# Kernel tuning notes

Measured on AMD Instinct MI355X. Metric: run time of the kernel, lower is better.

The kernel has to match this reference:

```python
import jax, jax.numpy as jnp
import numpy as np

B, S, D, H, MEL = 64, 512, 512, 8, 80
HD = D // H  # head dim


def _lstm_cell(x, h, c, w_ih, w_hh, b_ih, b_hh):
    # torch gate order: i, f, g, o
    gates = x @ w_ih.T + h @ w_hh.T + b_ih + b_hh
    i, f, g, o = jnp.split(gates, 4, axis=-1)
    c = jax.nn.sigmoid(f) * c + jax.nn.sigmoid(i) * jnp.tanh(g)
    h = jax.nn.sigmoid(o) * jnp.tanh(c)
    return h, c


def setup_inputs() -> dict:
    key = jax.random.key(0)
    ks = jax.random.split(key, 24)
    s = 0.05
    inp = {"encoder_output": jax.random.normal(ks[0], (B, S, D), jnp.float32)}
    # MultiheadAttention params (torch layout: in_proj [3D, D])
    inp["attn_in_w"] = jax.random.normal(ks[1], (3 * D, D), jnp.float32) * s
    inp["attn_in_b"] = jax.random.normal(ks[2], (3 * D,), jnp.float32) * s
    inp["attn_out_w"] = jax.random.normal(ks[3], (D, D), jnp.float32) * s
    inp["attn_out_b"] = jax.random.normal(ks[4], (D,), jnp.float32) * s
    # LSTM1 (2 layers)
    names = [("l1_w_ih0", (4 * D, D)), ("l1_w_hh0", (4 * D, D)), ("l1_b_ih0", (4 * D,)), ("l1_b_hh0", (4 * D,)),
             ("l1_w_ih1", (4 * D, D)), ("l1_w_hh1", (4 * D, D)), ("l1_b_ih1", (4 * D,)), ("l1_b_hh1", (4 * D,)),
             ("l2_w_ih", (4 * D, D)), ("l2_w_hh", (4 * D, D)), ("l2_b_ih", (4 * D,)), ("l2_b_hh", (4 * D,)),
             ("proj_w", (MEL, D)), ("proj_b", (MEL,))]
    for i, (n, shp) in enumerate(names):
        inp[n] = jax.random.normal(ks[5 + i], shp, jnp.float32) * s
    return inp


def reference(encoder_output, attn_in_w, attn_in_b, attn_out_w, attn_out_b,
              l1_w_ih0, l1_w_hh0, l1_b_ih0, l1_b_hh0,
              l1_w_ih1, l1_w_hh1, l1_b_ih1, l1_b_hh1,
              l2_w_ih, l2_w_hh, l2_b_ih, l2_b_hh, proj_w, proj_b):
    b, s, d = encoder_output.shape
    max_len = s * 5
    wq, wk, wv = jnp.split(attn_in_w, 3, axis=0)
    bq, bk, bv = jnp.split(attn_in_b, 3, axis=0)
    # Precompute K, V over encoder output: [B, S, H, HD]
    K = (encoder_output @ wk.T + bk).reshape(b, s, H, HD)
    V = (encoder_output @ wv.T + bv).reshape(b, s, H, HD)
    scale = 1.0 / np.sqrt(HD)

    def attend(x):  # x: [B, D] single-token query
        q = ((x @ wq.T + bq) * scale).reshape(b, H, HD)
        scores = jnp.einsum('bhd,bshd->bhs', q, K)
        w = jax.nn.softmax(scores, axis=-1)
        ctx = jnp.einsum('bhs,bshd->bhd', w, V).reshape(b, d)
        return ctx @ attn_out_w.T + attn_out_b

    zeros = jnp.zeros((b, d), encoder_output.dtype)
    carry0 = (zeros, zeros, zeros, zeros, zeros, zeros, zeros)

    def step(carry, _):
        h10, c10, h11, c11, h2, c2, dec_in = carry
        h10, c10 = _lstm_cell(dec_in, h10, c10, l1_w_ih0, l1_w_hh0, l1_b_ih0, l1_b_hh0)
        h11, c11 = _lstm_cell(h10, h11, c11, l1_w_ih1, l1_w_hh1, l1_b_ih1, l1_b_hh1)
        attn_out = attend(h11)
        h2, c2 = _lstm_cell(attn_out, h2, c2, l2_w_ih, l2_w_hh, l2_b_ih, l2_b_hh)
        out = h2 @ proj_w.T + proj_b  # [B, MEL]
        return (h10, c10, h11, c11, h2, c2, h2), out

    _, ys = jax.lax.scan(step, carry0, None, length=max_len)
    return jnp.transpose(ys, (1, 0, 2))  # [B, max_len, MEL]
```

## Files before the change

### kernel.cpp

```cpp
#include <hip/hip_runtime.h>
#include <hip/hip_bf16.h>
#include <hip/hip_fp8.h>

#define DEV_INLINE __device__ __forceinline__

typedef __attribute__((ext_vector_type(8))) short bf16x8;
typedef __attribute__((ext_vector_type(4))) float f32x4;
typedef __attribute__((ext_vector_type(2))) float f32x2;
typedef __attribute__((ext_vector_type(4))) unsigned int u32x4;
typedef unsigned long long ull;

constexpr int Bc = 64, Sc = 512, Dc = 512, Hc = 8, HDc = 64, MELc = 80, Tc = 2560;
constexpr int OUTSTRIDE = Tc * MELc;

constexpr size_t SZ_KP8 = 64ull * 8 * 512 * 64;
constexpr size_t SZ_VP  = 64ull * 8 * 512 * 64 * 2;
constexpr size_t SZ_PL  = 128ull * 2048 * 16;
constexpr size_t OFF_KP8 = 0;
constexpr size_t OFF_VP  = OFF_KP8 + SZ_KP8;
constexpr size_t OFF_PL0 = OFF_VP + SZ_VP;
constexpr size_t OFF_PL1 = OFF_PL0 + SZ_PL;
constexpr size_t OFF_PL2 = OFF_PL1 + SZ_PL;
constexpr size_t OFF_PWQ = OFF_PL2 + SZ_PL;
constexpr size_t OFF_PP  = OFF_PWQ + 524288;
constexpr size_t OFF_BL0 = OFF_PP + 81920;
constexpr size_t OFF_BL1 = OFF_BL0 + 8192;
constexpr size_t OFF_BL2 = OFF_BL1 + 8192;
constexpr size_t OFF_B2E = OFF_BL2 + 8192;
constexpr size_t OFF_W2E = OFF_B2E + 8192;
constexpr size_t OFF_WOT = OFF_W2E + 2097152;
constexpr size_t OFF_ACT = OFF_WOT + 1048576;
constexpr size_t OFF_FLG = OFF_ACT + 524288;

constexpr unsigned DYN_LDS = 121088;

DEV_INLINE float bf2f(short s) { return __uint_as_float(((unsigned)(unsigned short)s) << 16); }
DEV_INLINE short f2bf(float f) { union { __hip_bfloat16 h; short s; } u; u.h = __float2bfloat16(f); return u.s; }
DEV_INLINE float sig_f(float x) { return 1.0f / (1.0f + __expf(-x)); }
DEV_INLINE float tanh_f(float x) {
  float ax = fabsf(x);
  float e = __expf(fminf(2.0f * ax, 80.0f));
  float r = 1.0f - 2.0f / (e + 1.0f);
  return copysignf(r, x);
}
DEV_INLINE bf16x8 cvt8(const float* p) {
  bf16x8 r;
#pragma unroll
  for (int i = 0; i < 8; ++i) r[i] = f2bf(p[i]);
  return r;
}
DEV_INLINE float fp8tof(unsigned v) {
  __hip_fp8_e4m3 t; t.__x = (__hip_fp8_storage_t)v; return (float)t;
}

template <bool HI>
DEV_INLINE f32x2 cvt2_fp8(unsigned w) {
#if defined(__has_builtin) && __has_builtin(__builtin_amdgcn_cvt_pk_f32_fp8)
  return __builtin_amdgcn_cvt_pk_f32_fp8(w, HI);
#else
  unsigned b = HI ? (w >> 16) : w;
  f32x2 r; r[0] = fp8tof(b & 0xFFu); r[1] = fp8tof((b >> 8) & 0xFFu);
  return r;
#endif
}

DEV_INLINE ull ld_dev_u64(const void* p) {
  return __hip_atomic_load((const ull*)p, __ATOMIC_RELAXED, __HIP_MEMORY_SCOPE_AGENT);
}
DEV_INLINE void st_dev_u64(void* p, ull v) {
  __hip_atomic_store((ull*)p, v, __ATOMIC_RELAXED, __HIP_MEMORY_SCOPE_AGENT);
}
DEV_INLINE bf16x8 ld_frag(const __hip_bfloat16* p) {
  union { bf16x8 v; ull u[2]; } r;
  r.u[0] = ld_dev_u64(p);
  r.u[1] = ld_dev_u64((const char*)p + 8);
  return r.v;
}

__global__ __launch_bounds__(256) void gemm_setup(const float* __restrict__ A,
                                                  const float* __restrict__ Bt,
                                                  const float* __restrict__ bias,
                                                  __hip_bfloat16* __restrict__ dst,
                                                  unsigned char* __restrict__ dst8,
                                                  int mode) {
  int tid = threadIdx.x, lane = tid & 63, wv = tid >> 6;
  int m0 = blockIdx.y * 64 + wv * 16;
  int nb = blockIdx.x * 64;
  int mrow = m0 + (lane & 15);
  int kb = (lane >> 4) * 8;
  f32x4 acc0 = {0,0,0,0}, acc1 = {0,0,0,0}, acc2 = {0,0,0,0}, acc3 = {0,0,0,0};
  const float* arow = A + (size_t)mrow * 512 + kb;
  const float* b0r = Bt + (size_t)(nb + 0 * 16 + (lane & 15)) * 512 + kb;
  const float* b1r = Bt + (size_t)(nb + 1 * 16 + (lane & 15)) * 512 + kb;
  const float* b2r = Bt + (size_t)(nb + 2 * 16 + (lane & 15)) * 512 + kb;
  const float* b3r = Bt + (size_t)(nb + 3 * 16 + (lane & 15)) * 512 + kb;
  for (int kk = 0; kk < 16; ++kk) {
    bf16x8 af = cvt8(arow + kk * 32);
    acc0 = __builtin_amdgcn_mfma_f32_16x16x32_bf16(af, cvt8(b0r + kk * 32), acc0, 0, 0, 0);
    acc1 = __builtin_amdgcn_mfma_f32_16x16x32_bf16(af, cvt8(b1r + kk * 32), acc1, 0, 0, 0);
    acc2 = __builtin_amdgcn_mfma_f32_16x16x32_bf16(af, cvt8(b2r + kk * 32), acc2, 0, 0, 0);
    acc3 = __builtin_amdgcn_mfma_f32_16x16x32_bf16(af, cvt8(b3r + kk * 32), acc3, 0, 0, 0);
  }
  int col16 = lane & 15, r0 = (lane >> 4) * 4;
  f32x4 accs[4] = {acc0, acc1, acc2, acc3};
#pragma unroll
  for (int nt = 0; nt < 4; ++nt) {
    int n = nb + nt * 16 + col16;
#pragma unroll
    for (int r = 0; r < 4; ++r) {
      int m = m0 + r0 + r;
      float v = accs[nt][r];
      if (mode == 0) {
        v += bias[n];
        int bb = m >> 9, s = m & 511, h = n >> 6, d = n & 63;
        dst[(((size_t)(bb * 8 + h) * 512 + s) * 64) + d] = __float2bfloat16(v);
      } else if (mode == 2) {
        v += bias[n];
        int bb = m >> 9, s = m & 511, h = n >> 6, d = n & 63;
        __hip_fp8_e4m3 q(v);
        dst8[(((size_t)(bb * 8 + h) * 512 + s) * 64) + d] = (unsigned char)q.__x;
      } else {
        dst[(size_t)m * 512 + n] = __float2bfloat16(v);
      }
    }
  }
}

__global__ __launch_bounds__(256) void transpose512(const float* __restrict__ in, float* __restrict__ out) {
  __shared__ float tl[32][33];
  int x = threadIdx.x & 31, ty = threadIdx.x >> 5;
  int bx = blockIdx.x * 32, by = blockIdx.y * 32;
#pragma unroll
  for (int r = 0; r < 4; ++r) tl[ty + r * 8][x] = in[(size_t)(by + ty + r * 8) * 512 + bx + x];
  __syncthreads();
#pragma unroll
  for (int r = 0; r < 4; ++r) out[(size_t)(bx + ty + r * 8) * 512 + by + x] = tl[x][ty + r * 8];
}

__global__ __launch_bounds__(256) void b2eff_k(const float* __restrict__ w2ih, const float* __restrict__ bout,
                                               const float* __restrict__ bih, const float* __restrict__ bhh,
                                               float* __restrict__ dst) {
  int g = blockIdx.x * 256 + threadIdx.x;
  float acc = bih[g] + bhh[g];
  const float* row = w2ih + (size_t)g * 512;
  for (int k = 0; k < 512; ++k) acc += row[k] * bout[k];
  dst[g] = acc;
}

__global__ __launch_bounds__(256) void pack_lstm(const float* __restrict__ lo_f32,
                                                 const __hip_bfloat16* __restrict__ lo_bf16,
                                                 const float* __restrict__ hi_f32,
                                                 const float* __restrict__ b1, const float* __restrict__ b2,
                                                 const float* __restrict__ b_pre,
                                                 __hip_bfloat16* __restrict__ dst, float* __restrict__ bias_out,
                                                 int mode) {
  int u = blockIdx.x, tid = threadIdx.x;
  for (int rep = 0; rep < 8; ++rep) {
    int slot = rep * 256 + tid;
    int kk = slot >> 6, lane = slot & 63;
    int n16 = lane & 15, gate = n16 >> 2, jj = n16 & 3;
    int srow = gate * 512 + u * 4 + jj;
    int k = kk * 32 + (lane >> 4) * 8;
    __hip_bfloat16 tmp[8];
    if (k < 512) {
      if (mode == 0) {
#pragma unroll
        for (int i = 0; i < 8; ++i) tmp[i] = __float2bfloat16(lo_f32[(size_t)srow * 512 + k + i]);
      } else {
#pragma unroll
        for (int i = 0; i < 8; ++i) tmp[i] = lo_bf16[(size_t)srow * 512 + k + i];
      }
    } else {
#pragma unroll
      for (int i = 0; i < 8; ++i) tmp[i] = __float2bfloat16(hi_f32[(size_t)srow * 512 + (k - 512) + i]);
    }
    *(uint4*)(dst + ((size_t)u * 2048 + slot) * 8) = *(uint4*)tmp;
  }
  if (tid < 16) {
    int gate = tid >> 2, jj = tid & 3;
    int srow = gate * 512 + u * 4 + jj;
    bias_out[u * 16 + tid] = (mode == 0) ? (b1[srow] + b2[srow]) : b_pre[srow];
  }
}

__global__ __launch_bounds__(256) void pack_wq(const float* __restrict__ wq, __hip_bfloat16* __restrict__ dst) {
  int h = blockIdx.x, tid = threadIdx.x;
  for (int rep = 0; rep < 16; ++rep) {
    int slot = rep * 256 + tid;
    int nt = slot >> 10, kk = (slot >> 6) & 15, lane = slot & 63;
    int srow = h * 64 + nt * 16 + (lane & 15);
    int k = kk * 32 + (lane >> 4) * 8;
    __hip_bfloat16 tmp[8];
#pragma unroll
    for (int i = 0; i < 8; ++i) tmp[i] = __float2bfloat16(wq[(size_t)srow * 512 + k + i]);
    *(uint4*)(dst + ((size_t)h * 4096 + slot) * 8) = *(uint4*)tmp;
  }
}

struct DecParams {
  const float* attn_in_b;
  const float* proj_b;
  const float* proj_w;
  const uint4* packL0; const uint4* packL1; const uint4* packL2;
  const float* biasL0; const float* biasL1; const float* biasL2;
  const uint4* packWq;
  const unsigned char* Kp8; const __hip_bfloat16* Vp;
  __hip_bfloat16* h10b; __hip_bfloat16* h11b; __hip_bfloat16* h2b; __hip_bfloat16* ctxb;
  ull* actbase;
  unsigned* flags;
  float* out;
};

constexpr ull WD_TICKS = 200000000ull;

DEV_INLINE unsigned* ctrp(unsigned* f, int g, int s, int h) {
  return f + 32 + (((g << 2) + s) * 2 + h) * 32;
}

DEV_INLINE void publish_ctr(unsigned* c, int tid) {
  __builtin_amdgcn_s_waitcnt(0);
  __syncthreads();
  if (tid == 0)
    (void)__hip_atomic_fetch_add(c, 1u, __ATOMIC_RELAXED, __HIP_MEMORY_SCOPE_AGENT);
}

DEV_INLINE bool wait_ctr(unsigned* c, unsigned target, ull t0, int* sbail) {
  for (;;) {
    unsigned v = (unsigned)__builtin_amdgcn_readfirstlane(
        (int)__hip_atomic_load(c, __ATOMIC_RELAXED, __HIP_MEMORY_SCOPE_AGENT));
    if (v >= target) return true;
    if (__builtin_amdgcn_s_memrealtime() - t0 > WD_TICKS) { *sbail = 1; return false; }
    __builtin_amdgcn_s_sleep(1);
  }
}

DEV_INLINE void prefetch_hi(bf16x8* pf, const __hip_bfloat16* hi, int g, int lane, int wv) {
  if (wv >= 2) {
    const __hip_bfloat16* p = hi + (size_t)(g * 32 + (wv & 1) * 16 + (lane & 15)) * 512 + (lane >> 4) * 8;
#pragma unroll
    for (int kk = 0; kk < 16; ++kk) pf[kk] = ld_frag(p + kk * 32);
  }
}

DEV_INLINE bool lstm_stage(int tid, int g, int wgl,
                           const uint4* wlds, const float* bias,
                           const __hip_bfloat16* lo, const bf16x8* pf,
                           float* cstate, __hip_bfloat16* hc,
                           float* pred, ull* st64,
                           unsigned* c_lo, unsigned* c_hi, unsigned target,
                           ull t0, int* sbail) {
  const int lane = tid & 63, wv = tid >> 6, mt = wv & 1, kh = wv >> 1;
  f32x4 acc = {0,0,0,0};
  if (kh == 0) {
    const __hip_bfloat16* pA = lo + (size_t)(g * 32 + mt * 16 + (lane & 15)) * 512 + (lane >> 4) * 8;
    if (wait_ctr(c_lo, target, t0, sbail)) {
#pragma unroll
      for (int kk = 0; kk < 8; ++kk) {
        bf16x8 a = ld_frag(pA + kk * 32);
        bf16x8 b = *(const bf16x8*)(wlds + kk * 64 + lane);
        acc = __builtin_amdgcn_mfma_f32_16x16x32_bf16(a, b, acc, 0, 0, 0);
      }
      if (wait_ctr(c_hi, target, t0, sbail)) {
#pragma unroll
        for (int kk = 8; kk < 16; ++kk) {
          bf16x8 a = ld_frag(pA + kk * 32);
          bf16x8 b = *(const bf16x8*)(wlds + kk * 64 + lane);
          acc = __builtin_amdgcn_mfma_f32_16x16x32_bf16(a, b, acc, 0, 0, 0);
        }
      }
    }
  } else {
#pragma unroll
    for (int kk = 0; kk < 16; ++kk) {
      bf16x8 b = *(const bf16x8*)(wlds + (16 + kk) * 64 + lane);
      acc = __builtin_amdgcn_mfma_f32_16x16x32_bf16(pf[kk], b, acc, 0, 0, 0);
    }
  }
#pragma unroll
  for (int r = 0; r < 4; ++r) pred[wv * 256 + lane * 4 + r] = acc[r];
  __syncthreads();
  if (*sbail) return false;
  if (tid < 128) {
    int bl = tid >> 2, j = tid & 3;
    int mt2 = bl >> 4, qd = (bl & 15) >> 2, reg = bl & 3;
    const float* p0 = pred + mt2 * 256;
    const float* p1 = pred + (2 + mt2) * 256;
    int l0 = qd * 16;
    float gi = p0[(l0 + j) * 4 + reg]      + p1[(l0 + j) * 4 + reg]      + bias[j];
    float gf = p0[(l0 + 4 + j) * 4 + reg]  + p1[(l0 + 4 + j) * 4 + reg]  + bias[4 + j];
    float gg = p0[(l0 + 8 + j) * 4 + reg]  + p1[(l0 + 8 + j) * 4 + reg]  + bias[8 + j];
    float go = p0[(l0 + 12 + j) * 4 + reg] + p1[(l0 + 12 + j) * 4 + reg] + bias[12 + j];
    float c = cstate[tid & 127];
    c = sig_f(gf) * c + sig_f(gi) * tanh_f(gg);
    float h = sig_f(go) * tanh_f(c);
    cstate[tid & 127] = c;
    ((unsigned short*)st64)[tid] = (unsigned short)f2bf(h);
  }
  __syncthreads();
  if (tid < 32)
    st_dev_u64(hc + (size_t)(g * 32 + tid) * 512 + wgl * 4, st64[tid]);
  return true;
}

DEV_INLINE void proj_spread(int tid, int g, int wgl, const float* pw, const float* pb,
                            const __hip_bfloat16* h2in, float* outp) {
  const int lane = tid & 63, pr = tid >> 6;
#pragma unroll
  for (int r = 0; r < 5; ++r) {
    int P = wgl * 20 + r * 4 + pr;
    int b = P / 80, m = P - b * 80;
    bf16x8 hv = ld_frag(h2in + (size_t)(g * 32 + b) * 512 + lane * 8);
    const f32x4* w4 = (const f32x4*)(pw + (size_t)m * 512 + lane * 8);
    f32x4 wa = w4[0], wb = w4[1];
    float acc = bf2f(hv[0]) * wa[0] + bf2f(hv[1]) * wa[1] + bf2f(hv[2]) * wa[2] + bf2f(hv[3]) * wa[3]
              + bf2f(hv[4]) * wb[0] + bf2f(hv[5]) * wb[1] + bf2f(hv[6]) * wb[2] + bf2f(hv[7]) * wb[3];
#pragma unroll
    for (int off = 32; off; off >>= 1) acc += __shfl_xor(acc, off);
    if (lane == 0) outp[(size_t)(g * 32 + b) * OUTSTRIDE + m] = acc + pb[m];
  }
}

__global__ __launch_bounds__(256, 1) void decoder_main(DecParams P) {
  extern __shared__ char smem[];
  uint4* wL0 = (uint4*)smem;
  uint4* wL1 = wL0 + 2048;
  uint4* wL2 = wL1 + 2048;
  ull*   st64 = (ull*)(wL2 + 2048);
  float* pred = (float*)(st64 + 32);
  float* qls  = pred + 1024;
  float* sco  = qls + 1088;
  float* red  = sco + 1024;
  float* cst  = red + 2048;
  float* smx  = cst + 384;
  float* ssum = smx + 4;
  float* sinv = ssum + 4;
  int*   sbail = (int*)(sinv + 2);

  const int wg = blockIdx.x, tid = threadIdx.x;
  const int lane = tid & 63, wv = tid >> 6;
  const int g = wg >> 7;
  const int wgl = wg & 127;
  const int myhalf = wgl >> 6;
  const int hh = wgl >> 4;
  const int b0g = (wgl & 15) * 2;
  const int bblk = b0g & ~15;

  const ull t0 = __builtin_amdgcn_s_memrealtime();
  unsigned* F = P.flags;

  {
    const uint4* s0 = P.packL0 + (size_t)wgl * 2048;
    const uint4* s1 = P.packL1 + (size_t)wgl * 2048;
    const uint4* s2 = P.packL2 + (size_t)wgl * 2048;
    for (int i = tid; i < 2048; i += 256) { wL0[i] = s0[i]; wL1[i] = s1[i]; wL2[i] = s2[i]; }
  }
  if (tid == 0) *sbail = 0;
  if (tid < 128) { cst[tid] = 0.0f; cst[128 + tid] = 0.0f; cst[256 + tid] = 0.0f; }
  st_dev_u64(P.actbase + (size_t)wg * 256 + tid, 0ull);
  __syncthreads();
  publish_ctr(F, tid);
  if (!wait_ctr(F, 256u, t0, sbail)) goto bail;
  __syncthreads();

  for (int t = 0; t < Tc; ++t) {
    const int cur = t & 1, pv = cur ^ 1;
    const unsigned tgtP = 64u * (unsigned)t;
    const unsigned tgtC = 64u * (unsigned)(t + 1);
    __hip_bfloat16* h10c = P.h10b + cur * 32768; __hip_bfloat16* h10p = P.h10b + pv * 32768;
    __hip_bfloat16* h11c = P.h11b + cur * 32768; __hip_bfloat16* h11p = P.h11b + pv * 32768;
    __hip_bfloat16* h2c  = P.h2b  + cur * 32768; __hip_bfloat16* h2p  = P.h2b  + pv * 32768;
    __hip_bfloat16* ctxc = P.ctxb + cur * 32768;

    {
      bf16x8 pf[16];
      prefetch_hi(pf, h10p, g, lane, wv);
      if (!lstm_stage(tid, g, wgl, wL0, P.biasL0 + wgl * 16, h2p, pf, cst, h10c, pred, st64,
                      ctrp(F, g, 3, 0), ctrp(F, g, 3, 1), tgtP, t0, sbail)) goto bail;
      publish_ctr(ctrp(F, g, 0, myhalf), tid);
    }
    if (t > 0)
      proj_spread(tid, g, wgl, P.proj_w, P.proj_b, h2p, P.out + (size_t)(t - 1) * MELc);

    {
      bf16x8 pf[16];
      prefetch_hi(pf, h11p, g, lane, wv);
      if (!lstm_stage(tid, g, wgl, wL1, P.biasL1 + wgl * 16, h10c, pf, cst + 128, h11c, pred, st64,
                      ctrp(F, g, 0, 0), ctrp(F, g, 0, 1), tgtC, t0, sbail)) goto bail;
      publish_ctr(ctrp(F, g, 1, myhalf), tid);
    }

    {
      int mrow = g * 32 + bblk + (lane & 15);
      const __hip_bfloat16* pA = h11c + (size_t)mrow * 512 + (lane >> 4) * 8;
      const uint4* pB = P.packWq + (size_t)hh * 4096 + wv * 1024;
      f32x4 acc = {0,0,0,0};
      if (wait_ctr(ctrp(F, g, 1, 0), tgtC, t0, sbail)) {
#pragma unroll
        for (int kk = 0; kk < 8; ++kk) {
          bf16x8 a = ld_frag(pA + kk * 32);
          bf16x8 b = *(const bf16x8*)(pB + kk * 64 + lane);
          acc = __builtin_amdgcn_mfma_f32_16x16x32_bf16(a, b, acc, 0, 0, 0);
        }
        if (wait_ctr(ctrp(F, g, 1, 1), tgtC, t0, sbail)) {
#pragma unroll
          for (int kk = 8; kk < 16; ++kk) {
            bf16x8 a = ld_frag(pA + kk * 32);
            bf16x8 b = *(const bf16x8*)(pB + kk * 64 + lane);
            acc = __builtin_amdgcn_mfma_f32_16x16x32_bf16(a, b, acc, 0, 0, 0);
          }
        }
      }
      int col = lane & 15, row0 = (lane >> 4) << 2;
      int dg = wv * 16 + col;
      float bq = P.attn_in_b[hh * 64 + dg];
#pragma unroll
      for (int r = 0; r < 4; ++r) qls[(row0 + r) * 68 + dg] = (acc[r] + bq) * 0.125f;
    }
    __syncthreads();
    if (*sbail) goto bail;
    {
      int p = tid >> 7, si = tid & 127;
      int bg = g * 32 + b0g + p;
      const float* qv = qls + ((b0g & 15) + p) * 68;
      f32x4 q4[16];
#pragma unroll
      for (int i = 0; i < 16; ++i) q4[i] = *(const f32x4*)(qv + 4 * i);
      const u32x4* Kb = (const u32x4*)(P.Kp8 + (size_t)(bg * 8 + hh) * 512 * 64);
#pragma unroll
      for (int ss = 0; ss < 4; ++ss) {
        int s = si * 4 + ss;
        const u32x4* kr = Kb + s * 4;
        f32x2 acc2 = {0.0f, 0.0f};
#pragma unroll
        for (int i = 0; i < 4; ++i) {
          u32x4 kv = kr[i];
#pragma unroll
          for (int j = 0; j < 4; ++j) {
            unsigned w = kv[j];
            f32x2 c01 = cvt2_fp8<false>(w);
            f32x2 c23 = cvt2_fp8<true>(w);
            f32x4 qq = q4[i * 4 + j];
            acc2 += c01 * (f32x2){qq[0], qq[1]} + c23 * (f32x2){qq[2], qq[3]};
          }
        }
        sco[p * 512 + s] = acc2[0] + acc2[1];
      }
    }
    __syncthreads();
    {
      int p = wv >> 1, half = wv & 1;
      int idx = tid & 127;
      float mx = -1e30f;
#pragma unroll
      for (int ss = 0; ss < 4; ++ss) mx = fmaxf(mx, sco[p * 512 + idx * 4 + ss]);
#pragma unroll
      for (int off = 32; off; off >>= 1) mx = fmaxf(mx, __shfl_xor(mx, off));
      if (lane == 0) smx[p * 2 + half] = mx;
      __syncthreads();
      float m = fmaxf(smx[p * 2], smx[p * 2 + 1]);
      float sum = 0.0f;
#pragma unroll
      for (int ss = 0; ss < 4; ++ss) {
        int ix = p * 512 + idx * 4 + ss;
        float e = __expf(sco[ix] - m);
        sco[ix] = e; sum += e;
      }
#pragma unroll
      for (int off = 32; off; off >>= 1) sum += __shfl_xor(sum, off);
      if (lane == 0) ssum[p * 2 + half] = sum;
      __syncthreads();
      if (tid < 2) sinv[tid] = 1.0f / (ssum[tid * 2] + ssum[tid * 2 + 1]);
    }
    __syncthreads();
    {
      int p = wv >> 1, half = wv & 1;
      int bg = g * 32 + b0g + p;
      int sg = lane >> 3, dj = lane & 7;
      const char* Vb = (const char*)(P.Vp + (size_t)(bg * 8 + hh) * 512 * 64);
      f32x2 aA[4] = {{0,0},{0,0},{0,0},{0,0}};
      f32x2 aB[4] = {{0,0},{0,0},{0,0},{0,0}};
      const int s0 = half * 256 + sg;
#pragma unroll 8
      for (int it = 0; it < 16; ++it) {
        int sA = s0 + it * 8, sB = sA + 128;
        const char* pa = Vb + (size_t)sA * 128 + dj * 16;
        const char* pq = Vb + (size_t)sB * 128 + dj * 16;
        ull a0 = ld_dev_u64(pa), a1 = ld_dev_u64(pa + 8);
        ull b0 = ld_dev_u64(pq), b1 = ld_dev_u64(pq + 8);
        float wa = sco[p * 512 + sA], wb = sco[p * 512 + sB];
        f32x2 wA = {wa, wa}, wB = {wb, wb};
        unsigned va[4] = {(unsigned)a0, (unsigned)(a0 >> 32), (unsigned)a1, (unsigned)(a1 >> 32)};
        unsigned vb[4] = {(unsigned)b0, (unsigned)(b0 >> 32), (unsigned)b1, (unsigned)(b1 >> 32)};
#pragma unroll
        for (int j = 0; j < 4; ++j) {
          f32x2 fa = { __uint_as_float(va[j] << 16), __uint_as_float(va[j] & 0xFFFF0000u) };
          f32x2 fb = { __uint_as_float(vb[j] << 16), __uint_as_float(vb[j] & 0xFFFF0000u) };
          aA[j] += wA * fa;
          aB[j] += wB * fb;
        }
      }
      float* rp = red + ((p * 16 + half * 8 + sg) * 64) + dj * 8;
#pragma unroll
      for (int j = 0; j < 4; ++j) {
        rp[j * 2]     = aA[j][0] + aB[j][0];
        rp[j * 2 + 1] = aA[j][1] + aB[j][1];
      }
    }
    __syncthreads();
    if (tid < 128) {
      int p = tid >> 6, d = tid & 63;
      float sacc = 0.0f;
#pragma unroll
      for (int k = 0; k < 16; ++k) sacc += red[(p * 16 + k) * 64 + d];
      sacc *= sinv[p];
      ((unsigned short*)st64)[tid] = (unsigned short)f2bf(sacc);
    }
    __syncthreads();
    if (tid < 32) {
      int p = tid >> 4, q = tid & 15;
      st_dev_u64(ctxc + (size_t)(g * 32 + b0g + p) * 512 + hh * 64 + q * 4, st64[p * 16 + q]);
    }
    publish_ctr(ctrp(F, g, 2, myhalf), tid);

    {
      bf16x8 pf[16];
      prefetch_hi(pf, h2p, g, lane, wv);
      if (!lstm_stage(tid, g, wgl, wL2, P.biasL2 + wgl * 16, ctxc, pf, cst + 256, h2c, pred, st64,
                      ctrp(F, g, 2, 0), ctrp(F, g, 2, 1), tgtC, t0, sbail)) goto bail;
      publish_ctr(ctrp(F, g, 3, myhalf), tid);
    }
  }

  if (wait_ctr(ctrp(F, g, 3, 0), 64u * Tc, t0, sbail) &&
      wait_ctr(ctrp(F, g, 3, 1), 64u * Tc, t0, sbail)) {
    __syncthreads();
    proj_spread(tid, g, wgl, P.proj_w, P.proj_b, P.h2b + ((Tc - 1) & 1) * 32768,
                P.out + (size_t)(Tc - 1) * MELc);
  }
  return;

bail:
  if (tid == 0) {
    (void)__hip_atomic_fetch_add(F, 1u << 20, __ATOMIC_RELAXED, __HIP_MEMORY_SCOPE_AGENT);
    for (int gg = 0; gg < 2; ++gg)
      for (int s = 0; s < 4; ++s)
        for (int h = 0; h < 2; ++h)
          (void)__hip_atomic_fetch_add(ctrp(F, gg, s, h), 1u << 20,
                                       __ATOMIC_RELAXED, __HIP_MEMORY_SCOPE_AGENT);
  }
}

extern "C" void kernel_launch(void* const* d_in, const int* in_sizes, int n_in,
                              void* d_out, int out_size, void* d_ws, size_t ws_size,
                              hipStream_t stream) {
  const float* enc        = (const float*)d_in[0];
  const float* attn_in_w  = (const float*)d_in[1];
  const float* attn_in_b  = (const float*)d_in[2];
  const float* attn_out_w = (const float*)d_in[3];
  const float* attn_out_b = (const float*)d_in[4];
  const float* w_ih0 = (const float*)d_in[5];
  const float* w_hh0 = (const float*)d_in[6];
  const float* b_ih0 = (const float*)d_in[7];
  const float* b_hh0 = (const float*)d_in[8];
  const float* w_ih1 = (const float*)d_in[9];
  const float* w_hh1 = (const float*)d_in[10];
  const float* b_ih1 = (const float*)d_in[11];
  const float* b_hh1 = (const float*)d_in[12];
  const float* w_ih2 = (const float*)d_in[13];
  const float* w_hh2 = (const float*)d_in[14];
  const float* b_ih2 = (const float*)d_in[15];
  const float* b_hh2 = (const float*)d_in[16];
  const float* proj_w = (const float*)d_in[17];
  const float* proj_b = (const float*)d_in[18];

  char* ws = (char*)d_ws;
  unsigned char*  Kp8 = (unsigned char*)(ws + OFF_KP8);
  __hip_bfloat16* Vp  = (__hip_bfloat16*)(ws + OFF_VP);
  __hip_bfloat16* pl0 = (__hip_bfloat16*)(ws + OFF_PL0);
  __hip_bfloat16* pl1 = (__hip_bfloat16*)(ws + OFF_PL1);
  __hip_bfloat16* pl2 = (__hip_bfloat16*)(ws + OFF_PL2);
  __hip_bfloat16* pwq = (__hip_bfloat16*)(ws + OFF_PWQ);
  float* bl0 = (float*)(ws + OFF_BL0);
  float* bl1 = (float*)(ws + OFF_BL1);
  float* bl2 = (float*)(ws + OFF_BL2);
  float* b2e = (float*)(ws + OFF_B2E);
  __hip_bfloat16* w2e = (__hip_bfloat16*)(ws + OFF_W2E);
  float* wot = (float*)(ws + OFF_WOT);
  char* act  = ws + OFF_ACT;
  unsigned* flags = (unsigned*)(ws + OFF_FLG);

  hipMemsetAsync(flags, 0, 4096, stream);

  gemm_setup<<<dim3(8, 512), 256, 0, stream>>>(enc, attn_in_w + 512 * 512, attn_in_b + 512, nullptr, Kp8, 2);
  gemm_setup<<<dim3(8, 512), 256, 0, stream>>>(enc, attn_in_w + 1024 * 512, attn_in_b + 1024, Vp, nullptr, 0);
  transpose512<<<dim3(16, 16), 256, 0, stream>>>(attn_out_w, wot);
  gemm_setup<<<dim3(8, 32), 256, 0, stream>>>(w_ih2, wot, nullptr, w2e, nullptr, 1);
  b2eff_k<<<8, 256, 0, stream>>>(w_ih2, attn_out_b, b_ih2, b_hh2, b2e);
  pack_lstm<<<128, 256, 0, stream>>>(w_ih0, nullptr, w_hh0, b_ih0, b_hh0, nullptr, pl0, bl0, 0);
  pack_lstm<<<128, 256, 0, stream>>>(w_ih1, nullptr, w_hh1, b_ih1, b_hh1, nullptr, pl1, bl1, 0);
  pack_lstm<<<128, 256, 0, stream>>>(nullptr, w2e, w_hh2, nullptr, nullptr, b2e, pl2, bl2, 1);
  pack_wq<<<8, 256, 0, stream>>>(attn_in_w, pwq);

  DecParams p;
  p.attn_in_b = attn_in_b;
  p.proj_b = proj_b;
  p.proj_w = proj_w;
  p.packL0 = (const uint4*)pl0; p.packL1 = (const uint4*)pl1; p.packL2 = (const uint4*)pl2;
  p.biasL0 = bl0; p.biasL1 = bl1; p.biasL2 = bl2;
  p.packWq = (const uint4*)pwq;
  p.Kp8 = Kp8; p.Vp = Vp;
  p.h10b = (__hip_bfloat16*)(act + 0);
  p.h11b = (__hip_bfloat16*)(act + 131072);
  p.h2b  = (__hip_bfloat16*)(act + 262144);
  p.ctxb = (__hip_bfloat16*)(act + 393216);
  p.actbase = (ull*)act;
  p.flags = flags;
  p.out = (float*)d_out;

  (void)hipFuncSetAttribute((const void*)decoder_main,
                            hipFuncAttributeMaxDynamicSharedMemorySize, DYN_LDS);
  decoder_main<<<dim3(256), dim3(256), DYN_LDS, stream>>>(p);
}
```

Before: 106.0 ms.

## Shard step counters across cache lines and prefetch V before softmax

Each half-group counter, formerly incremented by 64 workgroups, is split into eight sub-counters on separate 128-byte lines, each taking 8 increments. Waiters poll all eight with one wave-wide load and an all-lanes check. The intent is to cut atomic contention on hot lines in the per-step grid barrier. Separately, the V tile loads for the context reduction now start right after the scores are computed, before the softmax barrier, so their latency overlaps the softmax. That costs 64 extra 64-bit registers per thread and may hurt occupancy or cause spills.

```diff
diff --git a/kernel.cpp b/kernel.cpp
--- a/kernel.cpp
+++ b/kernel.cpp
@@ -22,15 +22,14 @@
 constexpr size_t OFF_PL1 = OFF_PL0 + SZ_PL;
 constexpr size_t OFF_PL2 = OFF_PL1 + SZ_PL;
 constexpr size_t OFF_PWQ = OFF_PL2 + SZ_PL;
-constexpr size_t OFF_PP  = OFF_PWQ + 524288;
-constexpr size_t OFF_BL0 = OFF_PP + 81920;
+constexpr size_t OFF_CTR = OFF_PWQ + 524288;
+constexpr size_t OFF_BL0 = OFF_CTR + 81920;
 constexpr size_t OFF_BL1 = OFF_BL0 + 8192;
 constexpr size_t OFF_BL2 = OFF_BL1 + 8192;
 constexpr size_t OFF_B2E = OFF_BL2 + 8192;
 constexpr size_t OFF_W2E = OFF_B2E + 8192;
 constexpr size_t OFF_WOT = OFF_W2E + 2097152;
 constexpr size_t OFF_ACT = OFF_WOT + 1048576;
-constexpr size_t OFF_FLG = OFF_ACT + 524288;
 
 constexpr unsigned DYN_LDS = 121088;
 
@@ -213,18 +212,26 @@
 
 constexpr ull WD_TICKS = 200000000ull;
 
-DEV_INLINE unsigned* ctrp(unsigned* f, int g, int s, int h) {
-  return f + 32 + (((g << 2) + s) * 2 + h) * 32;
-}
-
-DEV_INLINE void publish_ctr(unsigned* c, int tid) {
+DEV_INLINE int ctr_idx(int g, int s, int h) { return (((g << 2) + s) * 2 + h) * 8; }
+
+DEV_INLINE void publish8(unsigned* F, int line, int tid) {
   __builtin_amdgcn_s_waitcnt(0);
   __syncthreads();
   if (tid == 0)
-    (void)__hip_atomic_fetch_add(c, 1u, __ATOMIC_RELAXED, __HIP_MEMORY_SCOPE_AGENT);
-}
-
-DEV_INLINE bool wait_ctr(unsigned* c, unsigned target, ull t0, int* sbail) {
+    (void)__hip_atomic_fetch_add(F + line * 32, 1u, __ATOMIC_RELAXED, __HIP_MEMORY_SCOPE_AGENT);
+}
+
+DEV_INLINE bool wait8(unsigned* F, int idx, unsigned target, int lane, ull t0, int* sbail) {
+  unsigned* p = F + (idx + (lane & 7)) * 32;
+  for (;;) {
+    unsigned v = __hip_atomic_load(p, __ATOMIC_RELAXED, __HIP_MEMORY_SCOPE_AGENT);
+    if (__all(v >= target ? 1 : 0)) return true;
+    if (__builtin_amdgcn_s_memrealtime() - t0 > WD_TICKS) { *sbail = 1; return false; }
+    __builtin_amdgcn_s_sleep(1);
+  }
+}
+
+DEV_INLINE bool wait_one(unsigned* c, unsigned target, ull t0, int* sbail) {
   for (;;) {
     unsigned v = (unsigned)__builtin_amdgcn_readfirstlane(
         (int)__hip_atomic_load(c, __ATOMIC_RELAXED, __HIP_MEMORY_SCOPE_AGENT));
@@ -247,20 +254,20 @@
                            const __hip_bfloat16* lo, const bf16x8* pf,
                            float* cstate, __hip_bfloat16* hc,
                            float* pred, ull* st64,
-                           unsigned* c_lo, unsigned* c_hi, unsigned target,
+                           unsigned* F, int idx, unsigned target,
                            ull t0, int* sbail) {
   const int lane = tid & 63, wv = tid >> 6, mt = wv & 1, kh = wv >> 1;
   f32x4 acc = {0,0,0,0};
   if (kh == 0) {
     const __hip_bfloat16* pA = lo + (size_t)(g * 32 + mt * 16 + (lane & 15)) * 512 + (lane >> 4) * 8;
-    if (wait_ctr(c_lo, target, t0, sbail)) {
+    if (wait8(F, idx, target, lane, t0, sbail)) {
 #pragma unroll
       for (int kk = 0; kk < 8; ++kk) {
         bf16x8 a = ld_frag(pA + kk * 32);
         bf16x8 b = *(const bf16x8*)(wlds + kk * 64 + lane);
         acc = __builtin_amdgcn_mfma_f32_16x16x32_bf16(a, b, acc, 0, 0, 0);
       }
-      if (wait_ctr(c_hi, target, t0, sbail)) {
+      if (wait8(F, idx + 8, target, lane, t0, sbail)) {
 #pragma unroll
         for (int kk = 8; kk < 16; ++kk) {
           bf16x8 a = ld_frag(pA + kk * 32);
@@ -341,6 +348,7 @@
   const int g = wg >> 7;
   const int wgl = wg & 127;
   const int myhalf = wgl >> 6;
+  const int mysub = (wgl >> 3) & 7;
   const int hh = wgl >> 4;
   const int b0g = (wgl & 15) * 2;
   const int bblk = b0g & ~15;
@@ -358,14 +366,14 @@
   if (tid < 128) { cst[tid] = 0.0f; cst[128 + tid] = 0.0f; cst[256 + tid] = 0.0f; }
   st_dev_u64(P.actbase + (size_t)wg * 256 + tid, 0ull);
   __syncthreads();
-  publish_ctr(F, tid);
-  if (!wait_ctr(F, 256u, t0, sbail)) goto bail;
+  publish8(F, 128, tid);
+  if (!wait_one(F + 128 * 32, 256u, t0, sbail)) goto bail;
   __syncthreads();
 
   for (int t = 0; t < Tc; ++t) {
     const int cur = t & 1, pv = cur ^ 1;
-    const unsigned tgtP = 64u * (unsigned)t;
-    const unsigned tgtC = 64u * (unsigned)(t + 1);
+    const unsigned tgtP = 8u * (unsigned)t;
+    const unsigned tgtC = 8u * (unsigned)(t + 1);
     __hip_bfloat16* h10c = P.h10b + cur * 32768; __hip_bfloat16* h10p = P.h10b + pv * 32768;
     __hip_bfloat16* h11c = P.h11b + cur * 32768; __hip_bfloat16* h11p = P.h11b + pv * 32768;
     __hip_bfloat16* h2c  = P.h2b  + cur * 32768; __hip_bfloat16* h2p  = P.h2b  + pv * 32768;
@@ -375,8 +383,8 @@
       bf16x8 pf[16];
       prefetch_hi(pf, h10p, g, lane, wv);
       if (!lstm_stage(tid, g, wgl, wL0, P.biasL0 + wgl * 16, h2p, pf, cst, h10c, pred, st64,
-                      ctrp(F, g, 3, 0), ctrp(F, g, 3, 1), tgtP, t0, sbail)) goto bail;
-      publish_ctr(ctrp(F, g, 0, myhalf), tid);
+                      F, ctr_idx(g, 3, 0), tgtP, t0, sbail)) goto bail;
+      publish8(F, ctr_idx(g, 0, myhalf) + mysub, tid);
     }
     if (t > 0)
       proj_spread(tid, g, wgl, P.proj_w, P.proj_b, h2p, P.out + (size_t)(t - 1) * MELc);
@@ -385,23 +393,25 @@
       bf16x8 pf[16];
       prefetch_hi(pf, h11p, g, lane, wv);
       if (!lstm_stage(tid, g, wgl, wL1, P.biasL1 + wgl * 16, h10c, pf, cst + 128, h11c, pred, st64,
-                      ctrp(F, g, 0, 0), ctrp(F, g, 0, 1), tgtC, t0, sbail)) goto bail;
-      publish_ctr(ctrp(F, g, 1, myhalf), tid);
-    }
+                      F, ctr_idx(g, 0, 0), tgtC, t0, sbail)) goto bail;
+      publish8(F, ctr_idx(g, 1, myhalf) + mysub, tid);
+    }
+
+    ull va0[16], va1[16], vb0[16], vb1[16];
 
     {
       int mrow = g * 32 + bblk + (lane & 15);
       const __hip_bfloat16* pA = h11c + (size_t)mrow * 512 + (lane >> 4) * 8;
       const uint4* pB = P.packWq + (size_t)hh * 4096 + wv * 1024;
       f32x4 acc = {0,0,0,0};
-      if (wait_ctr(ctrp(F, g, 1, 0), tgtC, t0, sbail)) {
+      if (wait8(F, ctr_idx(g, 1, 0), tgtC, lane, t0, sbail)) {
 #pragma unroll
         for (int kk = 0; kk < 8; ++kk) {
           bf16x8 a = ld_frag(pA + kk * 32);
           bf16x8 b = *(const bf16x8*)(pB + kk * 64 + lane);
           acc = __builtin_amdgcn_mfma_f32_16x16x32_bf16(a, b, acc, 0, 0, 0);
         }
-        if (wait_ctr(ctrp(F, g, 1, 1), tgtC, t0, sbail)) {
+        if (wait8(F, ctr_idx(g, 1, 1), tgtC, lane, t0, sbail)) {
 #pragma unroll
           for (int kk = 8; kk < 16; ++kk) {
             bf16x8 a = ld_frag(pA + kk * 32);
@@ -445,6 +455,21 @@
         }
         sco[p * 512 + s] = acc2[0] + acc2[1];
       }
+      {
+        int pp = wv >> 1, hf = wv & 1;
+        int bgp = g * 32 + b0g + pp;
+        int sg = lane >> 3, dj = lane & 7;
+        const char* Vb = (const char*)(P.Vp + (size_t)(bgp * 8 + hh) * 512 * 64);
+        const int s0v = hf * 256 + sg;
+#pragma unroll
+        for (int it = 0; it < 16; ++it) {
+          const char* pa = Vb + (size_t)(s0v + it * 8) * 128 + dj * 16;
+          const char* pq = Vb + (size_t)(s0v + it * 8 + 128) * 128 + dj * 16;
+          va0[it] = ld_dev_u64(pa); va1[it] = ld_dev_u64(pa + 8);
+          vb0[it] = ld_dev_u64(pq); vb1[it] = ld_dev_u64(pq + 8);
+        }
+        asm volatile("" ::: "memory");
+      }
     }
     __syncthreads();
     {
@@ -474,23 +499,19 @@
     __syncthreads();
     {
       int p = wv >> 1, half = wv & 1;
-      int bg = g * 32 + b0g + p;
       int sg = lane >> 3, dj = lane & 7;
-      const char* Vb = (const char*)(P.Vp + (size_t)(bg * 8 + hh) * 512 * 64);
       f32x2 aA[4] = {{0,0},{0,0},{0,0},{0,0}};
       f32x2 aB[4] = {{0,0},{0,0},{0,0},{0,0}};
       const int s0 = half * 256 + sg;
-#pragma unroll 8
+#pragma unroll
       for (int it = 0; it < 16; ++it) {
         int sA = s0 + it * 8, sB = sA + 128;
-        const char* pa = Vb + (size_t)sA * 128 + dj * 16;
-        const char* pq = Vb + (size_t)sB * 128 + dj * 16;
-        ull a0 = ld_dev_u64(pa), a1 = ld_dev_u64(pa + 8);
-        ull b0 = ld_dev_u64(pq), b1 = ld_dev_u64(pq + 8);
         float wa = sco[p * 512 + sA], wb = sco[p * 512 + sB];
         f32x2 wA = {wa, wa}, wB = {wb, wb};
-        unsigned va[4] = {(unsigned)a0, (unsigned)(a0 >> 32), (unsigned)a1, (unsigned)(a1 >> 32)};
-        unsigned vb[4] = {(unsigned)b0, (unsigned)(b0 >> 32), (unsigned)b1, (unsigned)(b1 >> 32)};
+        unsigned va[4] = {(unsigned)va0[it], (unsigned)(va0[it] >> 32),
+                          (unsigned)va1[it], (unsigned)(va1[it] >> 32)};
+        unsigned vb[4] = {(unsigned)vb0[it], (unsigned)(vb0[it] >> 32),
+                          (unsigned)vb1[it], (unsigned)(vb1[it] >> 32)};
 #pragma unroll
         for (int j = 0; j < 4; ++j) {
           f32x2 fa = { __uint_as_float(va[j] << 16), __uint_as_float(va[j] & 0xFFFF0000u) };
@@ -520,19 +541,19 @@
       int p = tid >> 4, q = tid & 15;
       st_dev_u64(ctxc + (size_t)(g * 32 + b0g + p) * 512 + hh * 64 + q * 4, st64[p * 16 + q]);
     }
-    publish_ctr(ctrp(F, g, 2, myhalf), tid);
+    publish8(F, ctr_idx(g, 2, myhalf) + mysub, tid);
 
     {
       bf16x8 pf[16];
       prefetch_hi(pf, h2p, g, lane, wv);
       if (!lstm_stage(tid, g, wgl, wL2, P.biasL2 + wgl * 16, ctxc, pf, cst + 256, h2c, pred, st64,
-                      ctrp(F, g, 2, 0), ctrp(F, g, 2, 1), tgtC, t0, sbail)) goto bail;
-      publish_ctr(ctrp(F, g, 3, myhalf), tid);
-    }
-  }
-
-  if (wait_ctr(ctrp(F, g, 3, 0), 64u * Tc, t0, sbail) &&
-      wait_ctr(ctrp(F, g, 3, 1), 64u * Tc, t0, sbail)) {
+                      F, ctr_idx(g, 2, 0), tgtC, t0, sbail)) goto bail;
+      publish8(F, ctr_idx(g, 3, myhalf) + mysub, tid);
+    }
+  }
+
+  if (wait8(F, ctr_idx(g, 3, 0), 8u * Tc, lane, t0, sbail) &&
+      wait8(F, ctr_idx(g, 3, 1), 8u * Tc, lane, t0, sbail)) {
     __syncthreads();
     proj_spread(tid, g, wgl, P.proj_w, P.proj_b, P.h2b + ((Tc - 1) & 1) * 32768,
                 P.out + (size_t)(Tc - 1) * MELc);
@@ -540,14 +561,9 @@
   return;
 
 bail:
-  if (tid == 0) {
-    (void)__hip_atomic_fetch_add(F, 1u << 20, __ATOMIC_RELAXED, __HIP_MEMORY_SCOPE_AGENT);
-    for (int gg = 0; gg < 2; ++gg)
-      for (int s = 0; s < 4; ++s)
-        for (int h = 0; h < 2; ++h)
-          (void)__hip_atomic_fetch_add(ctrp(F, gg, s, h), 1u << 20,
-                                       __ATOMIC_RELAXED, __HIP_MEMORY_SCOPE_AGENT);
-  }
+  if (tid == 0)
+    for (int i = 0; i <= 128; ++i)
+      (void)__hip_atomic_fetch_add(F + i * 32, 1u << 20, __ATOMIC_RELAXED, __HIP_MEMORY_SCOPE_AGENT);
 }
 
 extern "C" void kernel_launch(void* const* d_in, const int* in_sizes, int n_in,
@@ -587,9 +603,9 @@
   __hip_bfloat16* w2e = (__hip_bfloat16*)(ws + OFF_W2E);
   float* wot = (float*)(ws + OFF_WOT);
   char* act  = ws + OFF_ACT;
-  unsigned* flags = (unsigned*)(ws + OFF_FLG);
-
-  hipMemsetAsync(flags, 0, 4096, stream);
+  unsigned* ctrs = (unsigned*)(ws + OFF_CTR);
+
+  hipMemsetAsync(ctrs, 0, 20480, stream);
 
   gemm_setup<<<dim3(8, 512), 256, 0, stream>>>(enc, attn_in_w + 512 * 512, attn_in_b + 512, nullptr, Kp8, 2);
   gemm_setup<<<dim3(8, 512), 256, 0, stream>>>(enc, attn_in_w + 1024 * 512, attn_in_b + 1024, Vp, nullptr, 0);
@@ -614,7 +630,7 @@
   p.h2b  = (__hip_bfloat16*)(act + 262144);
   p.ctxb = (__hip_bfloat16*)(act + 393216);
   p.actbase = (ull*)act;
-  p.flags = flags;
+  p.flags = ctrs;
   p.out = (float*)d_out;
 
   (void)hipFuncSetAttribute((const void*)decoder_main,
```

Result: slower. 117.3 ms (+10.6%).
